# Kernel tuning notes

Measured on AMD Instinct MI355X. Metric: run time of the kernel, lower is better.

The kernel has to match this reference:

```python
import jax, jax.numpy as jnp
import numpy as np

NEG = -9e15  # matches torch's -9000000000000000.0 masking constant


def setup_inputs() -> dict:
    key = jax.random.key(0)
    kq, kk, kv, ka = jax.random.split(key, 4)
    B, H, N, d = 8, 8, 1024, 128
    queries = jax.random.normal(kq, (B, H, N, d), dtype=jnp.float32)
    keys = jax.random.normal(kk, (B, H, N, d), dtype=jnp.float32)
    values = jax.random.normal(kv, (B, H, N, d), dtype=jnp.float32)
    adj = jax.random.randint(ka, (N, N), 0, 2, dtype=jnp.int32)
    return {"queries": queries, "keys": keys, "values": values, "adj": adj}


def reference(queries, keys, values, adj):
    # scores: [B,H,N,N]; original divides by the constant 8 (not sqrt(dim))
    e = jnp.einsum("bhnd,bhmd->bhnm", queries, keys) / 8.0
    # adjacency mask [N,N] broadcasts over batch and heads
    att = jnp.where(adj > 0, e, jnp.asarray(NEG, e.dtype))
    att = jax.nn.softmax(att, axis=-1)
    # dropout is identity in eval mode
    h = jnp.einsum("bhnm,bhmd->bhnd", att, values)  # [B,H,N,d]
    B, H, N, d = h.shape
    # original uses .view (raw reshape), NOT a permute
    return jnp.reshape(h, (N, B, H, d))
```

## Files before the change

kernel.cpp:

```cpp
#include <hip/hip_runtime.h>
#include <hip/hip_bf16.h>


typedef __bf16 bf16x8 __attribute__((ext_vector_type(8)));
typedef float  f32x4  __attribute__((ext_vector_type(4)));
typedef unsigned int u32;

#define NSEQ 1024
#define DH   128
#define BN   64
#define NKT  16
#define TILE_ELEMS (BN * DH)
#define C1 0.1803368801111244f
#define C2 11.5415603271110070f

__device__ __forceinline__ float f4get(const float4& v, int c) {
    return (c == 0) ? v.x : (c == 1) ? v.y : (c == 2) ? v.z : v.w;
}

__device__ __forceinline__ void gload_lds16(const void* g, void* l) {
    __builtin_amdgcn_global_load_lds(
        (const __attribute__((address_space(1))) u32*)g,
        (__attribute__((address_space(3))) u32*)l, 16, 0, 0);
}

__global__ __launch_bounds__(256)
void prepack_kernel(const float* __restrict__ K, const float* __restrict__ V,
                    __bf16* __restrict__ Kws, __bf16* __restrict__ Vws)
{
    const int tid = threadIdx.x;
    const int id  = blockIdx.x;
    const size_t gbase = (size_t)(id >> 4) * NSEQ * DH + (size_t)(id & 15) * BN * DH;
    __bf16* ko = Kws + (size_t)id * TILE_ELEMS;
    __bf16* vo = Vws + (size_t)id * TILE_ELEMS;

    {
        const int r  = tid >> 2;
        const int c0 = (tid & 3) * 4;
        #pragma unroll
        for (int cc = 0; cc < 4; ++cc) {
            const int c = c0 + cc;
            const float* src = K + gbase + (size_t)r * DH + c * 8;
            float4 a = *(const float4*)src;
            float4 b = *(const float4*)(src + 4);
            bf16x8 w;
            w[0]=(__bf16)a.x; w[1]=(__bf16)a.y; w[2]=(__bf16)a.z; w[3]=(__bf16)a.w;
            w[4]=(__bf16)b.x; w[5]=(__bf16)b.y; w[6]=(__bf16)b.z; w[7]=(__bf16)b.w;
            const int cs = (c & 8) | ((c ^ (r & 7)) & 7);
            *(bf16x8*)(ko + r * DH + cs * 8) = w;
        }
    }
    {
        const int vkvb = tid >> 5;
        const int vdb  = tid & 31;
        float4 vr[8];
        #pragma unroll
        for (int rr = 0; rr < 8; ++rr)
            vr[rr] = *(const float4*)(V + gbase + (size_t)(vkvb * 8 + rr) * DH + vdb * 4);
        #pragma unroll
        for (int c = 0; c < 4; ++c) {
            const int d = vdb * 4 + c;
            bf16x8 w;
            #pragma unroll
            for (int j = 0; j < 8; ++j) w[j] = (__bf16)f4get(vr[j], c);
            const int cs = vkvb ^ (d & 7);
            *(bf16x8*)(vo + d * BN + cs * 8) = w;
        }
    }
}

__global__ __launch_bounds__(256, 2)
void attn_fast(const float* __restrict__ Q, const __bf16* __restrict__ Kws,
               const __bf16* __restrict__ Vws, const int* __restrict__ adj,
               float* __restrict__ out)
{
    __shared__ __attribute__((aligned(16))) __bf16 Kt[2][TILE_ELEMS];
    __shared__ __attribute__((aligned(16))) __bf16 Vt[TILE_ELEMS];
    __shared__ __attribute__((aligned(16))) __bf16 Ps[128 * 72];

    const int tid  = threadIdx.x;
    const int wave = tid >> 6;
    const int lane = tid & 63;
    const int n16  = lane & 15;
    const int quad = lane >> 4;
    const int m7   = n16 & 7;

    const int id = blockIdx.x;
    const int bh = (id & 7) * 8 + ((id >> 3) & 7);
    const int q0 = (id >> 6) * 128;
    const size_t base  = (size_t)bh * NSEQ * DH;
    const size_t tile0 = (size_t)(bh * NKT) * TILE_ELEMS;

    bf16x8 qf[2][4];
    #pragma unroll
    for (int rt = 0; rt < 2; ++rt)
        #pragma unroll
        for (int ks = 0; ks < 4; ++ks) {
            const float* src = Q + base + (size_t)(q0 + wave * 32 + rt * 16 + n16) * DH
                             + ks * 32 + quad * 8;
            float4 a = *(const float4*)src;
            float4 b = *(const float4*)(src + 4);
            bf16x8 w;
            w[0]=(__bf16)a.x; w[1]=(__bf16)a.y; w[2]=(__bf16)a.z; w[3]=(__bf16)a.w;
            w[4]=(__bf16)b.x; w[5]=(__bf16)b.y; w[6]=(__bf16)b.z; w[7]=(__bf16)b.w;
            qf[rt][ks] = w;
        }

    f32x4 o[2][8];
    #pragma unroll
    for (int rt = 0; rt < 2; ++rt)
        #pragma unroll
        for (int i = 0; i < 8; ++i) o[rt][i] = (f32x4){0.f, 0.f, 0.f, 0.f};
    float lp[2][4] = {{0.f,0.f,0.f,0.f},{0.f,0.f,0.f,0.f}};

    #pragma unroll
    for (int j = 0; j < 4; ++j) {
        const int off = wave * 2048 + j * 512;
        gload_lds16(Kws + tile0 + off + lane * 8, &Kt[0][off]);
    }

    for (int kt = 0; kt < NKT; ++kt) {
        const int kv0 = kt * BN;

        __builtin_amdgcn_sched_barrier(0);
        asm volatile("s_waitcnt vmcnt(0)" ::: "memory");
        __builtin_amdgcn_sched_barrier(0);
        __builtin_amdgcn_s_barrier();
        __builtin_amdgcn_sched_barrier(0);

        int am[2][4][4];
        #pragma unroll
        for (int rt = 0; rt < 2; ++rt)
            #pragma unroll
            for (int i = 0; i < 4; ++i)
                #pragma unroll
                for (int t = 0; t < 4; ++t)
                    am[rt][i][t] = adj[(size_t)(q0 + wave * 32 + rt * 16 + quad * 4 + i) * NSEQ
                                       + kv0 + t * 16 + n16];
        __builtin_amdgcn_sched_barrier(0);

        {
            const __bf16* vtile = Vws + tile0 + (size_t)kt * TILE_ELEMS;
            #pragma unroll
            for (int j = 0; j < 4; ++j) {
                const int off = wave * 2048 + j * 512;
                gload_lds16(vtile + off + lane * 8, &Vt[off]);
            }
        }
        __builtin_amdgcn_sched_barrier(0);

        {
            const int ktn = (kt + 1) & (NKT - 1);
            const __bf16* ktile = Kws + tile0 + (size_t)ktn * TILE_ELEMS;
            __bf16* kdst = &Kt[ktn & 1][0];
            #pragma unroll
            for (int j = 0; j < 4; ++j) {
                const int off = wave * 2048 + j * 512;
                gload_lds16(ktile + off + lane * 8, kdst + off);
            }
        }
        __builtin_amdgcn_sched_barrier(0);

        const __bf16* Kc = &Kt[kt & 1][0];
        float sc[2][4][4];
        __builtin_amdgcn_s_setprio(1);
        #pragma unroll
        for (int t = 0; t < 4; ++t) {
            f32x4 acc0 = (f32x4){0.f, 0.f, 0.f, 0.f};
            f32x4 acc1 = (f32x4){0.f, 0.f, 0.f, 0.f};
            #pragma unroll
            for (int ks = 0; ks < 4; ++ks) {
                const int c  = ks * 4 + quad;
                const int cs = (c & 8) | ((c ^ m7) & 7);
                bf16x8 bfr = *(const bf16x8*)(Kc + (t * 16 + n16) * DH + cs * 8);
                acc0 = __builtin_amdgcn_mfma_f32_16x16x32_bf16(qf[0][ks], bfr, acc0, 0, 0, 0);
                acc1 = __builtin_amdgcn_mfma_f32_16x16x32_bf16(qf[1][ks], bfr, acc1, 0, 0, 0);
            }
            #pragma unroll
            for (int i = 0; i < 4; ++i) { sc[0][t][i] = acc0[i]; sc[1][t][i] = acc1[i]; }
        }
        __builtin_amdgcn_s_setprio(0);

        #pragma unroll
        for (int rt = 0; rt < 2; ++rt)
            #pragma unroll
            for (int i = 0; i < 4; ++i) {
                const int prow = wave * 32 + rt * 16 + quad * 4 + i;
                float rowsum = 0.f;
                #pragma unroll
                for (int t = 0; t < 4; ++t) {
                    float p = exp2f(sc[rt][t][i] * C1 - C2);
                    p = (am[rt][i][t] > 0) ? p : 0.f;
                    rowsum += p;
                    Ps[prow * 72 + t * 16 + n16] = (__bf16)p;
                }
                lp[rt][i] += rowsum;
            }

        __builtin_amdgcn_sched_barrier(0);
        asm volatile("s_waitcnt vmcnt(4) lgkmcnt(0)" ::: "memory");
        __builtin_amdgcn_sched_barrier(0);
        __builtin_amdgcn_s_barrier();
        __builtin_amdgcn_sched_barrier(0);

        __builtin_amdgcn_s_setprio(1);
        #pragma unroll
        for (int ks = 0; ks < 2; ++ks) {
            bf16x8 pf0 = *(const bf16x8*)(&Ps[(wave * 32 + n16)      * 72 + ks * 32 + quad * 8]);
            bf16x8 pf1 = *(const bf16x8*)(&Ps[(wave * 32 + 16 + n16) * 72 + ks * 32 + quad * 8]);
            #pragma unroll
            for (int nt = 0; nt < 8; ++nt) {
                const int d  = nt * 16 + n16;
                const int cs = (ks * 4 + quad) ^ m7;
                bf16x8 vf = *(const bf16x8*)(&Vt[d * BN + cs * 8]);
                o[0][nt] = __builtin_amdgcn_mfma_f32_16x16x32_bf16(pf0, vf, o[0][nt], 0, 0, 0);
                o[1][nt] = __builtin_amdgcn_mfma_f32_16x16x32_bf16(pf1, vf, o[1][nt], 0, 0, 0);
            }
        }
        __builtin_amdgcn_s_setprio(0);
    }

    #pragma unroll
    for (int rt = 0; rt < 2; ++rt) {
        float linv[4];
        #pragma unroll
        for (int i = 0; i < 4; ++i) {
            float ls = lp[rt][i];
            ls += __shfl_xor(ls, 1);
            ls += __shfl_xor(ls, 2);
            ls += __shfl_xor(ls, 4);
            ls += __shfl_xor(ls, 8);
            linv[i] = 1.0f / fmaxf(ls, 1e-30f);
        }
        const int qrow = q0 + wave * 32 + rt * 16 + quad * 4;
        #pragma unroll
        for (int nt = 0; nt < 8; ++nt)
            #pragma unroll
            for (int i = 0; i < 4; ++i)
                out[base + (size_t)(qrow + i) * DH + nt * 16 + n16] = o[rt][nt][i] * linv[i];
    }
}

#define KS_STRIDE 136
#define VT_STRIDE 64
#define PS_STRIDE 72

__global__ __launch_bounds__(256, 4)
void attn_fallback(const float* __restrict__ Q, const float* __restrict__ K,
                   const float* __restrict__ V, const int* __restrict__ adj,
                   float* __restrict__ out)
{
    __shared__ __attribute__((aligned(16))) __bf16 KsP[BN * KS_STRIDE];
    __shared__ __attribute__((aligned(16))) __bf16 Vts[DH * VT_STRIDE];
    const int tid = threadIdx.x;
    const int wave = tid >> 6, lane = tid & 63, n16 = lane & 15, quad = lane >> 4;
    const int id = blockIdx.x;
    const int bh = (id & 7) * 8 + ((id >> 3) & 7);
    const int q0 = (id >> 6) * 64;
    const size_t base = (size_t)bh * NSEQ * DH;
    const int rp = tid >> 4, kcol = (tid & 15) * 8, db = tid & 31, kvb = tid >> 5;
    bf16x8 qf[4];
    #pragma unroll
    for (int ks = 0; ks < 4; ++ks) {
        const float* src = Q + base + (size_t)(q0 + wave * 16 + n16) * DH + ks * 32 + quad * 8;
        float4 a = *(const float4*)src; float4 b = *(const float4*)(src + 4);
        bf16x8 w;
        w[0]=(__bf16)a.x; w[1]=(__bf16)a.y; w[2]=(__bf16)a.z; w[3]=(__bf16)a.w;
        w[4]=(__bf16)b.x; w[5]=(__bf16)b.y; w[6]=(__bf16)b.z; w[7]=(__bf16)b.w;
        qf[ks] = w;
    }
    f32x4 o[8];
    #pragma unroll
    for (int i = 0; i < 8; ++i) o[i] = (f32x4){0.f, 0.f, 0.f, 0.f};
    float lp[4] = {0.f, 0.f, 0.f, 0.f};
    const int qrow = q0 + wave * 16 + quad * 4;
    for (int kt = 0; kt < NKT; ++kt) {
        const int kv0 = kt * BN;
        __syncthreads();
        #pragma unroll
        for (int it = 0; it < 4; ++it) {
            int row = 16 * it + rp;
            const float* src = K + base + (size_t)(kv0 + row) * DH + kcol;
            float4 a = *(const float4*)src; float4 b = *(const float4*)(src + 4);
            bf16x8 w;
            w[0]=(__bf16)a.x; w[1]=(__bf16)a.y; w[2]=(__bf16)a.z; w[3]=(__bf16)a.w;
            w[4]=(__bf16)b.x; w[5]=(__bf16)b.y; w[6]=(__bf16)b.z; w[7]=(__bf16)b.w;
            *(bf16x8*)(&KsP[row * KS_STRIDE + kcol]) = w;
        }
        {
            float4 vreg[8];
            #pragma unroll
            for (int rr = 0; rr < 8; ++rr)
                vreg[rr] = *(const float4*)(V + base + (size_t)(kv0 + kvb * 8 + rr) * DH + db * 4);
            #pragma unroll
            for (int c = 0; c < 4; ++c) {
                bf16x8 w;
                #pragma unroll
                for (int j = 0; j < 8; ++j) w[j] = (__bf16)f4get(vreg[j], c);
                int d = db * 4 + c, s = (d ^ (d >> 3)) & 7;
                *(bf16x8*)(&Vts[d * VT_STRIDE + ((kvb ^ s) << 3)]) = w;
            }
        }
        __syncthreads();
        int am[4][4];
        #pragma unroll
        for (int i = 0; i < 4; ++i)
            #pragma unroll
            for (int t = 0; t < 4; ++t)
                am[i][t] = adj[(size_t)(qrow + i) * NSEQ + kv0 + t * 16 + n16];
        float sc[4][4];
        #pragma unroll
        for (int t = 0; t < 4; ++t) {
            f32x4 acc = (f32x4){0.f, 0.f, 0.f, 0.f};
            #pragma unroll
            for (int ks = 0; ks < 4; ++ks) {
                bf16x8 bfr = *(const bf16x8*)(&KsP[(t * 16 + n16) * KS_STRIDE + ks * 32 + quad * 8]);
                acc = __builtin_amdgcn_mfma_f32_16x16x32_bf16(qf[ks], bfr, acc, 0, 0, 0);
            }
            #pragma unroll
            for (int i = 0; i < 4; ++i) sc[t][i] = acc[i];
        }
        __syncthreads();
        #pragma unroll
        for (int i = 0; i < 4; ++i) {
            const int prow = wave * 16 + quad * 4 + i;
            float rowsum = 0.f;
            #pragma unroll
            for (int t = 0; t < 4; ++t) {
                float p = exp2f(sc[t][i] * C1 - C2);
                p = (am[i][t] > 0) ? p : 0.f;
                rowsum += p;
                KsP[prow * PS_STRIDE + t * 16 + n16] = (__bf16)p;
            }
            lp[i] += rowsum;
        }
        #pragma unroll
        for (int ks = 0; ks < 2; ++ks) {
            bf16x8 pf = *(const bf16x8*)(&KsP[(wave * 16 + n16) * PS_STRIDE + ks * 32 + quad * 8]);
            #pragma unroll
            for (int nt = 0; nt < 8; ++nt) {
                int d = nt * 16 + n16, s = (d ^ (d >> 3)) & 7, kvbr = ks * 4 + quad;
                bf16x8 vf = *(const bf16x8*)(&Vts[d * VT_STRIDE + ((kvbr ^ s) << 3)]);
                o[nt] = __builtin_amdgcn_mfma_f32_16x16x32_bf16(pf, vf, o[nt], 0, 0, 0);
            }
        }
    }
    float linv[4];
    #pragma unroll
    for (int i = 0; i < 4; ++i) {
        float ls = lp[i];
        ls += __shfl_xor(ls, 1); ls += __shfl_xor(ls, 2);
        ls += __shfl_xor(ls, 4); ls += __shfl_xor(ls, 8);
        linv[i] = 1.0f / fmaxf(ls, 1e-30f);
    }
    #pragma unroll
    for (int nt = 0; nt < 8; ++nt)
        #pragma unroll
        for (int i = 0; i < 4; ++i)
            out[base + (size_t)(qrow + i) * DH + nt * 16 + n16] = o[nt][i] * linv[i];
}

extern "C" void kernel_launch(void* const* d_in, const int* in_sizes, int n_in,
                              void* d_out, int out_size, void* d_ws, size_t ws_size,
                              hipStream_t stream) {
    const float* Q   = (const float*)d_in[0];
    const float* K   = (const float*)d_in[1];
    const float* V   = (const float*)d_in[2];
    const int*   adj = (const int*)d_in[3];
    float* out = (float*)d_out;
    const size_t need = (size_t)2 * 64 * NKT * TILE_ELEMS * sizeof(__bf16);
    if (ws_size >= need) {
        __bf16* Kws = (__bf16*)d_ws;
        __bf16* Vws = Kws + (size_t)64 * NKT * TILE_ELEMS;
        prepack_kernel<<<1024, 256, 0, stream>>>(K, V, Kws, Vws);
        attn_fast<<<512, 256, 0, stream>>>(Q, Kws, Vws, adj, out);
    } else {
        attn_fallback<<<1024, 256, 0, stream>>>(Q, K, V, adj, out);
    }
}
```

Before: 199.7 us.

## Bit-pack adjacency mask in prepack and use 8-wave blocks with 16 rows per wave

The prepack kernel gains extra blocks that compress the int32 adjacency matrix into 64-bit bitmasks. The attention kernel loads each row's mask bits once, in place of reading 16 int32 mask values per row per KV tile from global memory. The attention block grows to 512 threads (8 waves, 16 query rows each) with launch bounds of 4, and each wave copies half as many K/V tile chunks. Each K/V tile in LDS is now shared by more waves, but each wave issues half as many MFMAs per tile load, which could expose more latency.

```diff
diff --git a/kernel.cpp b/kernel.cpp
--- a/kernel.cpp
+++ b/kernel.cpp
@@ -5,6 +5,7 @@
 typedef __bf16 bf16x8 __attribute__((ext_vector_type(8)));
 typedef float  f32x4  __attribute__((ext_vector_type(4)));
 typedef unsigned int u32;
+typedef unsigned long long u64;
 
 #define NSEQ 1024
 #define DH   128
@@ -26,10 +27,24 @@
 
 __global__ __launch_bounds__(256)
 void prepack_kernel(const float* __restrict__ K, const float* __restrict__ V,
-                    __bf16* __restrict__ Kws, __bf16* __restrict__ Vws)
+                    __bf16* __restrict__ Kws, __bf16* __restrict__ Vws,
+                    u64* __restrict__ adjp, const int* __restrict__ adj)
 {
     const int tid = threadIdx.x;
     const int id  = blockIdx.x;
+
+    if (id >= 1024) {
+        const int r = (id - 1024) * 16 + (tid >> 4);
+        const int c = tid & 15;
+        const int* row = adj + (size_t)r * NSEQ + c;
+        u64 w = 0;
+        #pragma unroll
+        for (int j = 0; j < 64; ++j)
+            w |= (u64)(row[j * 16] > 0) << j;
+        adjp[(size_t)r * 16 + c] = w;
+        return;
+    }
+
     const size_t gbase = (size_t)(id >> 4) * NSEQ * DH + (size_t)(id & 15) * BN * DH;
     __bf16* ko = Kws + (size_t)id * TILE_ELEMS;
     __bf16* vo = Vws + (size_t)id * TILE_ELEMS;
@@ -69,9 +84,9 @@
     }
 }
 
-__global__ __launch_bounds__(256, 2)
+__global__ __launch_bounds__(512, 4)
 void attn_fast(const float* __restrict__ Q, const __bf16* __restrict__ Kws,
-               const __bf16* __restrict__ Vws, const int* __restrict__ adj,
+               const __bf16* __restrict__ Vws, const u64* __restrict__ adjp,
                float* __restrict__ out)
 {
     __shared__ __attribute__((aligned(16))) __bf16 Kt[2][TILE_ELEMS];
@@ -90,60 +105,49 @@
     const int q0 = (id >> 6) * 128;
     const size_t base  = (size_t)bh * NSEQ * DH;
     const size_t tile0 = (size_t)(bh * NKT) * TILE_ELEMS;
-
-    bf16x8 qf[2][4];
-    #pragma unroll
-    for (int rt = 0; rt < 2; ++rt)
-        #pragma unroll
-        for (int ks = 0; ks < 4; ++ks) {
-            const float* src = Q + base + (size_t)(q0 + wave * 32 + rt * 16 + n16) * DH
-                             + ks * 32 + quad * 8;
-            float4 a = *(const float4*)src;
-            float4 b = *(const float4*)(src + 4);
-            bf16x8 w;
-            w[0]=(__bf16)a.x; w[1]=(__bf16)a.y; w[2]=(__bf16)a.z; w[3]=(__bf16)a.w;
-            w[4]=(__bf16)b.x; w[5]=(__bf16)b.y; w[6]=(__bf16)b.z; w[7]=(__bf16)b.w;
-            qf[rt][ks] = w;
-        }
-
-    f32x4 o[2][8];
-    #pragma unroll
-    for (int rt = 0; rt < 2; ++rt)
-        #pragma unroll
-        for (int i = 0; i < 8; ++i) o[rt][i] = (f32x4){0.f, 0.f, 0.f, 0.f};
-    float lp[2][4] = {{0.f,0.f,0.f,0.f},{0.f,0.f,0.f,0.f}};
-
-    #pragma unroll
-    for (int j = 0; j < 4; ++j) {
-        const int off = wave * 2048 + j * 512;
+    const int qrb = q0 + wave * 16 + quad * 4;
+
+    bf16x8 qf[4];
+    #pragma unroll
+    for (int ks = 0; ks < 4; ++ks) {
+        const float* src = Q + base + (size_t)(q0 + wave * 16 + n16) * DH
+                         + ks * 32 + quad * 8;
+        float4 a = *(const float4*)src;
+        float4 b = *(const float4*)(src + 4);
+        bf16x8 w;
+        w[0]=(__bf16)a.x; w[1]=(__bf16)a.y; w[2]=(__bf16)a.z; w[3]=(__bf16)a.w;
+        w[4]=(__bf16)b.x; w[5]=(__bf16)b.y; w[6]=(__bf16)b.z; w[7]=(__bf16)b.w;
+        qf[ks] = w;
+    }
+
+    u64 aw[4];
+    #pragma unroll
+    for (int i = 0; i < 4; ++i)
+        aw[i] = adjp[(size_t)(qrb + i) * 16 + n16];
+
+    f32x4 o[8];
+    #pragma unroll
+    for (int i = 0; i < 8; ++i) o[i] = (f32x4){0.f, 0.f, 0.f, 0.f};
+    float lp[4] = {0.f, 0.f, 0.f, 0.f};
+
+    #pragma unroll
+    for (int j = 0; j < 2; ++j) {
+        const int off = wave * 1024 + j * 512;
         gload_lds16(Kws + tile0 + off + lane * 8, &Kt[0][off]);
     }
 
     for (int kt = 0; kt < NKT; ++kt) {
-        const int kv0 = kt * BN;
-
         __builtin_amdgcn_sched_barrier(0);
         asm volatile("s_waitcnt vmcnt(0)" ::: "memory");
         __builtin_amdgcn_sched_barrier(0);
         __builtin_amdgcn_s_barrier();
-        __builtin_amdgcn_sched_barrier(0);
-
-        int am[2][4][4];
-        #pragma unroll
-        for (int rt = 0; rt < 2; ++rt)
-            #pragma unroll
-            for (int i = 0; i < 4; ++i)
-                #pragma unroll
-                for (int t = 0; t < 4; ++t)
-                    am[rt][i][t] = adj[(size_t)(q0 + wave * 32 + rt * 16 + quad * 4 + i) * NSEQ
-                                       + kv0 + t * 16 + n16];
         __builtin_amdgcn_sched_barrier(0);
 
         {
             const __bf16* vtile = Vws + tile0 + (size_t)kt * TILE_ELEMS;
             #pragma unroll
-            for (int j = 0; j < 4; ++j) {
-                const int off = wave * 2048 + j * 512;
+            for (int j = 0; j < 2; ++j) {
+                const int off = wave * 1024 + j * 512;
                 gload_lds16(vtile + off + lane * 8, &Vt[off]);
             }
         }
@@ -154,51 +158,48 @@
             const __bf16* ktile = Kws + tile0 + (size_t)ktn * TILE_ELEMS;
             __bf16* kdst = &Kt[ktn & 1][0];
             #pragma unroll
-            for (int j = 0; j < 4; ++j) {
-                const int off = wave * 2048 + j * 512;
+            for (int j = 0; j < 2; ++j) {
+                const int off = wave * 1024 + j * 512;
                 gload_lds16(ktile + off + lane * 8, kdst + off);
             }
         }
         __builtin_amdgcn_sched_barrier(0);
 
         const __bf16* Kc = &Kt[kt & 1][0];
-        float sc[2][4][4];
+        float sc[4][4];
         __builtin_amdgcn_s_setprio(1);
         #pragma unroll
         for (int t = 0; t < 4; ++t) {
-            f32x4 acc0 = (f32x4){0.f, 0.f, 0.f, 0.f};
-            f32x4 acc1 = (f32x4){0.f, 0.f, 0.f, 0.f};
+            f32x4 acc = (f32x4){0.f, 0.f, 0.f, 0.f};
             #pragma unroll
             for (int ks = 0; ks < 4; ++ks) {
                 const int c  = ks * 4 + quad;
                 const int cs = (c & 8) | ((c ^ m7) & 7);
                 bf16x8 bfr = *(const bf16x8*)(Kc + (t * 16 + n16) * DH + cs * 8);
-                acc0 = __builtin_amdgcn_mfma_f32_16x16x32_bf16(qf[0][ks], bfr, acc0, 0, 0, 0);
-                acc1 = __builtin_amdgcn_mfma_f32_16x16x32_bf16(qf[1][ks], bfr, acc1, 0, 0, 0);
-            }
-            #pragma unroll
-            for (int i = 0; i < 4; ++i) { sc[0][t][i] = acc0[i]; sc[1][t][i] = acc1[i]; }
+                acc = __builtin_amdgcn_mfma_f32_16x16x32_bf16(qf[ks], bfr, acc, 0, 0, 0);
+            }
+            #pragma unroll
+            for (int i = 0; i < 4; ++i) sc[t][i] = acc[i];
         }
         __builtin_amdgcn_s_setprio(0);
 
         #pragma unroll
-        for (int rt = 0; rt < 2; ++rt)
-            #pragma unroll
-            for (int i = 0; i < 4; ++i) {
-                const int prow = wave * 32 + rt * 16 + quad * 4 + i;
-                float rowsum = 0.f;
-                #pragma unroll
-                for (int t = 0; t < 4; ++t) {
-                    float p = exp2f(sc[rt][t][i] * C1 - C2);
-                    p = (am[rt][i][t] > 0) ? p : 0.f;
-                    rowsum += p;
-                    Ps[prow * 72 + t * 16 + n16] = (__bf16)p;
-                }
-                lp[rt][i] += rowsum;
-            }
-
-        __builtin_amdgcn_sched_barrier(0);
-        asm volatile("s_waitcnt vmcnt(4) lgkmcnt(0)" ::: "memory");
+        for (int i = 0; i < 4; ++i) {
+            const unsigned w4 = (unsigned)(aw[i] >> (kt * 4)) & 0xFu;
+            const int prow = wave * 16 + quad * 4 + i;
+            float rowsum = 0.f;
+            #pragma unroll
+            for (int t = 0; t < 4; ++t) {
+                float p = exp2f(sc[t][i] * C1 - C2);
+                p = (w4 & (1u << t)) ? p : 0.f;
+                rowsum += p;
+                Ps[prow * 72 + t * 16 + n16] = (__bf16)p;
+            }
+            lp[i] += rowsum;
+        }
+
+        __builtin_amdgcn_sched_barrier(0);
+        asm volatile("s_waitcnt vmcnt(2) lgkmcnt(0)" ::: "memory");
         __builtin_amdgcn_sched_barrier(0);
         __builtin_amdgcn_s_barrier();
         __builtin_amdgcn_sched_barrier(0);
@@ -206,39 +207,33 @@
         __builtin_amdgcn_s_setprio(1);
         #pragma unroll
         for (int ks = 0; ks < 2; ++ks) {
-            bf16x8 pf0 = *(const bf16x8*)(&Ps[(wave * 32 + n16)      * 72 + ks * 32 + quad * 8]);
-            bf16x8 pf1 = *(const bf16x8*)(&Ps[(wave * 32 + 16 + n16) * 72 + ks * 32 + quad * 8]);
+            bf16x8 pf = *(const bf16x8*)(&Ps[(wave * 16 + n16) * 72 + ks * 32 + quad * 8]);
             #pragma unroll
             for (int nt = 0; nt < 8; ++nt) {
                 const int d  = nt * 16 + n16;
                 const int cs = (ks * 4 + quad) ^ m7;
                 bf16x8 vf = *(const bf16x8*)(&Vt[d * BN + cs * 8]);
-                o[0][nt] = __builtin_amdgcn_mfma_f32_16x16x32_bf16(pf0, vf, o[0][nt], 0, 0, 0);
-                o[1][nt] = __builtin_amdgcn_mfma_f32_16x16x32_bf16(pf1, vf, o[1][nt], 0, 0, 0);
+                o[nt] = __builtin_amdgcn_mfma_f32_16x16x32_bf16(pf, vf, o[nt], 0, 0, 0);
             }
         }
         __builtin_amdgcn_s_setprio(0);
     }
 
-    #pragma unroll
-    for (int rt = 0; rt < 2; ++rt) {
-        float linv[4];
-        #pragma unroll
-        for (int i = 0; i < 4; ++i) {
-            float ls = lp[rt][i];
-            ls += __shfl_xor(ls, 1);
-            ls += __shfl_xor(ls, 2);
-            ls += __shfl_xor(ls, 4);
-            ls += __shfl_xor(ls, 8);
-            linv[i] = 1.0f / fmaxf(ls, 1e-30f);
-        }
-        const int qrow = q0 + wave * 32 + rt * 16 + quad * 4;
-        #pragma unroll
-        for (int nt = 0; nt < 8; ++nt)
-            #pragma unroll
-            for (int i = 0; i < 4; ++i)
-                out[base + (size_t)(qrow + i) * DH + nt * 16 + n16] = o[rt][nt][i] * linv[i];
-    }
+    float linv[4];
+    #pragma unroll
+    for (int i = 0; i < 4; ++i) {
+        float ls = lp[i];
+        ls += __shfl_xor(ls, 1);
+        ls += __shfl_xor(ls, 2);
+        ls += __shfl_xor(ls, 4);
+        ls += __shfl_xor(ls, 8);
+        linv[i] = 1.0f / fmaxf(ls, 1e-30f);
+    }
+    #pragma unroll
+    for (int nt = 0; nt < 8; ++nt)
+        #pragma unroll
+        for (int i = 0; i < 4; ++i)
+            out[base + (size_t)(qrb + i) * DH + nt * 16 + n16] = o[nt][i] * linv[i];
 }
 
 #define KS_STRIDE 136
@@ -368,12 +363,14 @@
     const float* V   = (const float*)d_in[2];
     const int*   adj = (const int*)d_in[3];
     float* out = (float*)d_out;
-    const size_t need = (size_t)2 * 64 * NKT * TILE_ELEMS * sizeof(__bf16);
-    if (ws_size >= need) {
+    const size_t needKV  = (size_t)2 * 64 * NKT * TILE_ELEMS * sizeof(__bf16);
+    const size_t needAdj = (size_t)NSEQ * 16 * sizeof(u64);
+    if (ws_size >= needKV + needAdj) {
         __bf16* Kws = (__bf16*)d_ws;
         __bf16* Vws = Kws + (size_t)64 * NKT * TILE_ELEMS;
-        prepack_kernel<<<1024, 256, 0, stream>>>(K, V, Kws, Vws);
-        attn_fast<<<512, 256, 0, stream>>>(Q, Kws, Vws, adj, out);
+        u64* adjp = (u64*)(Vws + (size_t)64 * NKT * TILE_ELEMS);
+        prepack_kernel<<<1088, 256, 0, stream>>>(K, V, Kws, Vws, adjp, adj);
+        attn_fast<<<512, 512, 0, stream>>>(Q, Kws, Vws, adjp, out);
     } else {
         attn_fallback<<<1024, 256, 0, stream>>>(Q, K, V, adj, out);
     }
```

Measured after the change: 195.9 us. About the same (-1.9%).
